# Optimization experiments

Hardware: AMD Instinct MI355X
Metric: run time of the kernel (lower is better)

Reference implementation:

```python
import jax, jax.numpy as jnp
import numpy as np

# constants from init_kwargs (data_info / model_cfg)
FX = 300.0
FY = 300.0
CX = 128.0
CY = 128.0
BG = 1.0            # data_info['bg_color']
EPS2D = 0.3         # gsplat screen-space blur added to 2D covariance diagonal
NEAR = 0.01         # gsplat near-plane cull
C0 = 0.28209479177387814  # SH degree-0 basis
N_PTS = 512
IMG = 256


def quat_to_rotmat(q):
    # q: (N,4) wxyz, normalized inside
    q = q / jnp.linalg.norm(q, axis=-1, keepdims=True)
    w, x, y, z = q[:, 0], q[:, 1], q[:, 2], q[:, 3]
    return jnp.stack([
        jnp.stack([1 - 2 * (y * y + z * z), 2 * (x * y - w * z), 2 * (x * z + w * y)], -1),
        jnp.stack([2 * (x * y + w * z), 1 - 2 * (x * x + z * z), 2 * (y * z - w * x)], -1),
        jnp.stack([2 * (x * z - w * y), 2 * (y * z + w * x), 1 - 2 * (x * x + y * y)], -1),
    ], axis=-2)  # (N,3,3)


def setup_inputs() -> dict:
    key = jax.random.key(0)
    k = jax.random.split(key, 6)
    means = (jax.random.uniform(k[0], (N_PTS, 3), dtype=jnp.float32) - 0.5) * 10.0
    quats = jax.random.normal(k[1], (N_PTS, 4), dtype=jnp.float32)
    # log-scales around 0.2m so Gaussians actually cover pixels
    scales = jnp.log(0.2) + 0.1 * jax.random.normal(k[2], (N_PTS, 3), dtype=jnp.float32)
    opacities = jax.random.normal(k[3], (N_PTS,), dtype=jnp.float32)
    sh0 = 0.5 * jax.random.normal(k[4], (N_PTS, 1, 3), dtype=jnp.float32)
    shN = 0.01 * jax.random.normal(k[5], (N_PTS, 15, 3), dtype=jnp.float32)
    camtoworld = jnp.concatenate([jnp.eye(3, dtype=jnp.float32), jnp.zeros((3, 1), jnp.float32)], axis=1)
    return {"camtoworld": camtoworld, "means": means, "quats": quats, "scales": scales,
            "opacities": opacities, "sh0": sh0, "shN": shN, "img_h": IMG, "img_w": IMG}


def _render(camtoworld, means, quats, scales, opacities, sh0, shN, img_h, img_w):
    # --- camera setup (matches module forward) ---
    c2w = jnp.eye(4, dtype=jnp.float32).at[:3, :].set(camtoworld)
    viewmat = jnp.linalg.inv(c2w)
    viewmat = viewmat.at[1, :].multiply(-1.0).at[2, :].multiply(-1.0)
    R, t = viewmat[:3, :3], viewmat[:3, 3]

    # --- project means ---
    p = means @ R.T + t                      # (N,3) camera-space
    x, y, z = p[:, 0], p[:, 1], p[:, 2]
    valid = z > NEAR
    zs = jnp.where(valid, z, 1.0)
    rz = 1.0 / zs

    # --- 3D covariance: R(q) diag(s^2) R(q)^T, rotated to camera ---
    Rq = quat_to_rotmat(quats)
    M = Rq * jnp.exp(scales)[:, None, :]
    cov3d = M @ jnp.swapaxes(M, 1, 2)        # (N,3,3)
    cov_cam = jnp.einsum('ij,njk,lk->nil', R, cov3d, R)

    # --- EWA perspective Jacobian with fov clipping (gsplat persp_proj) ---
    limx = 1.3 * (0.5 * img_w / FX)
    limy = 1.3 * (0.5 * img_h / FY)
    tx = zs * jnp.clip(x * rz, -limx, limx)
    ty = zs * jnp.clip(y * rz, -limy, limy)
    zero = jnp.zeros_like(rz)
    J = jnp.stack([
        jnp.stack([FX * rz, zero, -FX * tx * rz * rz], -1),
        jnp.stack([zero, FY * rz, -FY * ty * rz * rz], -1),
    ], axis=1)                               # (N,2,3)
    cov2d = jnp.einsum('nij,njk,nlk->nil', J, cov_cam, J)
    a = cov2d[:, 0, 0] + EPS2D
    b = cov2d[:, 0, 1]
    c = cov2d[:, 1, 1] + EPS2D
    det = a * c - b * b
    valid = valid & (det > 1e-12)
    dets = jnp.where(valid, det, 1.0)
    cA, cB, cC = c / dets, -b / dets, a / dets   # conic (inverse 2D covariance)

    mx = FX * x * rz + CX
    my = FY * y * rz + CY

    # --- colors: sh_degree = 0 -> only sh0 band, clamped to >= 0 ---
    color = jnp.maximum(C0 * sh0[:, 0, :] + 0.5, 0.0)   # (N,3)
    opac = jax.nn.sigmoid(opacities)

    # --- depth sort (front to back) ---
    order = jnp.argsort(jnp.where(valid, z, jnp.inf))
    mx, my, cA, cB, cC, opac, color, valid = (v[order] for v in (mx, my, cA, cB, cC, opac, color, valid))

    # --- per-pixel alpha evaluation (dense [N,H,W]) ---
    px = jnp.arange(img_w, dtype=jnp.float32) + 0.5
    py = jnp.arange(img_h, dtype=jnp.float32) + 0.5
    dx = px[None, None, :] - mx[:, None, None]          # (N,H,W)
    dy = py[None, :, None] - my[:, None, None]
    sigma = 0.5 * (cA[:, None, None] * dx * dx + cC[:, None, None] * dy * dy) + cB[:, None, None] * dx * dy
    alpha = jnp.minimum(0.999, opac[:, None, None] * jnp.exp(-sigma))
    alpha = jnp.where((sigma >= 0.0) & (alpha >= 1.0 / 255.0) & valid[:, None, None], alpha, 0.0)

    # --- front-to-back alpha compositing via exclusive cumprod of (1-alpha) ---
    T = jnp.cumprod(1.0 - alpha, axis=0)                # (N,H,W)
    T_excl = jnp.concatenate([jnp.ones_like(T[:1]), T[:-1]], axis=0)
    w = T_excl * alpha
    render = jnp.einsum('nhw,nc->hwc', w, color) + T[-1][..., None] * BG   # (H,W,3)
    alpha_map = (1.0 - T[-1])[..., None]                                   # (H,W,1)
    return render, alpha_map


def reference(camtoworld, means, quats, scales, opacities, sh0, shN, img_h, img_w):
    return _render(camtoworld, means, quats, scales, opacities, sh0, shN, img_h, img_w)
```

## Files before the change

### kernel.cpp

```cpp
#include <hip/hip_runtime.h>
#include <math.h>

#define FXc 300.0f
#define FYc 300.0f
#define CXc 128.0f
#define CYc 128.0f
#define BGc 1.0f
#define EPS2Dc 0.3f
#define NEARc 0.01f
#define C0c 0.28209479177387814f

#define MAXP 512
#define SEG  4

__global__ void __launch_bounds__(1024)
gs_fused(const float* __restrict__ cam,
         const float* __restrict__ means,
         const float* __restrict__ quats,
         const float* __restrict__ scales,
         const float* __restrict__ opacs,
         const float* __restrict__ sh0,
         const int* __restrict__ img_w_p,
         float* __restrict__ out,
         int n, int npix)
{
    __shared__ float4 spts[MAXP][3];
    __shared__ __align__(16) float zc[MAXP + 4];
    __shared__ int scnt[MAXP / 64];
    __shared__ int sbase[MAXP / 64 + 1];
    __shared__ float4 comb[SEG - 1][256];

    const int lt   = threadIdx.x;
    const int wave = lt >> 6;

    const int W = *img_w_p;
    const int tiles_x = W >> 4;
    const int tx = (blockIdx.x % tiles_x) << 4;
    const int ty = (blockIdx.x / tiles_x) << 4;
    const float tx0 = (float)tx + 0.5f, tx1 = (float)tx + 15.5f;
    const float ty0 = (float)ty + 0.5f, ty1 = (float)ty + 15.5f;

    const int nchunks = (n + 63) >> 6;

    float pmx = 0.f, pmy = 0.f, pA_ = 0.f, pB_ = 0.f, pC_ = 0.f;
    float pop = 0.f, pcr = 0.f, pcg = 0.f, pcb = 0.f, pz = 0.f;
    unsigned long long mreg = 0ull;
    bool phit = false;

    if (lt < MAXP) {
        const float a00 = cam[0], a01 = cam[1], a02 = cam[2],  b0 = cam[3];
        const float a10 = cam[4], a11 = cam[5], a12 = cam[6],  b1 = cam[7];
        const float a20 = cam[8], a21 = cam[9], a22 = cam[10], b2 = cam[11];
        const float det3 = a00*(a11*a22 - a12*a21) - a01*(a10*a22 - a12*a20) + a02*(a10*a21 - a11*a20);
        const float id = 1.0f / det3;
        const float i00 = (a11*a22 - a12*a21)*id, i01 = (a02*a21 - a01*a22)*id, i02 = (a01*a12 - a02*a11)*id;
        const float i10 = (a12*a20 - a10*a22)*id, i11 = (a00*a22 - a02*a20)*id, i12 = (a02*a10 - a00*a12)*id;
        const float i20 = (a10*a21 - a11*a20)*id, i21 = (a01*a20 - a00*a21)*id, i22 = (a00*a11 - a01*a10)*id;
        const float R00 = i00,  R01 = i01,  R02 = i02;
        const float R10 = -i10, R11 = -i11, R12 = -i12;
        const float R20 = -i20, R21 = -i21, R22 = -i22;
        const float t0 = -(i00*b0 + i01*b1 + i02*b2);
        const float t1 = (i10*b0 + i11*b1 + i12*b2);
        const float t2 = (i20*b0 + i21*b1 + i22*b2);
        const float limx_e = 1.3f * (0.5f * (float)W / FXc);
        const float limy_e = limx_e;

        const int p = lt;
        bool hit = false;
        if (p < n) {
            const float m0 = means[3*p], m1 = means[3*p+1], m2 = means[3*p+2];
            const float px_ = R00*m0 + R01*m1 + R02*m2 + t0;
            const float py_ = R10*m0 + R11*m1 + R12*m2 + t1;
            const float pz_ = R20*m0 + R21*m1 + R22*m2 + t2;

            bool valid = pz_ > NEARc;
            const float zs = valid ? pz_ : 1.0f;
            const float rz = 1.0f / zs;

            float qw = quats[4*p], qx = quats[4*p+1], qy = quats[4*p+2], qz = quats[4*p+3];
            const float qn = rsqrtf(qw*qw + qx*qx + qy*qy + qz*qz);
            qw *= qn; qx *= qn; qy *= qn; qz *= qn;
            const float Rq00 = 1.f - 2.f*(qy*qy + qz*qz), Rq01 = 2.f*(qx*qy - qw*qz), Rq02 = 2.f*(qx*qz + qw*qy);
            const float Rq10 = 2.f*(qx*qy + qw*qz), Rq11 = 1.f - 2.f*(qx*qx + qz*qz), Rq12 = 2.f*(qy*qz - qw*qx);
            const float Rq20 = 2.f*(qx*qz - qw*qy), Rq21 = 2.f*(qy*qz + qw*qx), Rq22 = 1.f - 2.f*(qx*qx + qy*qy);

            const float e0 = __expf(scales[3*p]), e1 = __expf(scales[3*p+1]), e2 = __expf(scales[3*p+2]);
            const float M00 = Rq00*e0, M01 = Rq01*e1, M02 = Rq02*e2;
            const float M10 = Rq10*e0, M11 = Rq11*e1, M12 = Rq12*e2;
            const float M20 = Rq20*e0, M21 = Rq21*e1, M22 = Rq22*e2;

            const float S00 = M00*M00 + M01*M01 + M02*M02;
            const float S01 = M00*M10 + M01*M11 + M02*M12;
            const float S02 = M00*M20 + M01*M21 + M02*M22;
            const float S11 = M10*M10 + M11*M11 + M12*M12;
            const float S12 = M10*M20 + M11*M21 + M12*M22;
            const float S22 = M20*M20 + M21*M21 + M22*M22;

            const float U00 = R00*S00 + R01*S01 + R02*S02;
            const float U01 = R00*S01 + R01*S11 + R02*S12;
            const float U02 = R00*S02 + R01*S12 + R02*S22;
            const float U10 = R10*S00 + R11*S01 + R12*S02;
            const float U11 = R10*S01 + R11*S11 + R12*S12;
            const float U12 = R10*S02 + R11*S12 + R12*S22;
            const float U20 = R20*S00 + R21*S01 + R22*S02;
            const float U21 = R20*S01 + R21*S11 + R22*S12;
            const float U22 = R20*S02 + R21*S12 + R22*S22;

            const float C00 = U00*R00 + U01*R01 + U02*R02;
            const float C01 = U00*R10 + U01*R11 + U02*R12;
            const float C02 = U00*R20 + U01*R21 + U02*R22;
            const float C11 = U10*R10 + U11*R11 + U12*R12;
            const float C12 = U10*R20 + U11*R21 + U12*R22;
            const float C22 = U20*R20 + U21*R21 + U22*R22;

            const float txc = zs * fminf(fmaxf(px_*rz, -limx_e), limx_e);
            const float tyc = zs * fminf(fmaxf(py_*rz, -limy_e), limy_e);
            const float ja0 = FXc * rz;
            const float ja2 = -FXc * txc * rz * rz;
            const float jb1 = FYc * rz;
            const float jb2 = -FYc * tyc * rz * rz;

            const float c2d00 = ja0*ja0*C00 + 2.f*ja0*ja2*C02 + ja2*ja2*C22 + EPS2Dc;
            const float c2d01 = ja0*jb1*C01 + ja0*jb2*C02 + ja2*jb1*C12 + ja2*jb2*C22;
            const float c2d11 = jb1*jb1*C11 + 2.f*jb1*jb2*C12 + jb2*jb2*C22 + EPS2Dc;

            const float det2 = c2d00*c2d11 - c2d01*c2d01;
            valid = valid && (det2 > 1e-12f);
            const float rdet = 1.0f / (valid ? det2 : 1.0f);
            pA_ = c2d11 * rdet;
            pB_ = -c2d01 * rdet;
            pC_ = c2d00 * rdet;

            pmx = FXc * px_ * rz + CXc;
            pmy = FYc * py_ * rz + CYc;

            pcr = fmaxf(C0c * sh0[3*p+0] + 0.5f, 0.0f);
            pcg = fmaxf(C0c * sh0[3*p+1] + 0.5f, 0.0f);
            pcb = fmaxf(C0c * sh0[3*p+2] + 0.5f, 0.0f);
            pop = 1.0f / (1.0f + __expf(-opacs[p]));
            pz  = pz_;

            if (valid) {
                const float a_ = pA_, b_ = pB_, c_ = pC_;
                const float dx0 = tx0 - pmx, dx1 = tx1 - pmx;
                const float dy0 = ty0 - pmy, dy1 = ty1 - pmy;
                float smin;
                if (dx0 <= 0.f && 0.f <= dx1 && dy0 <= 0.f && 0.f <= dy1) {
                    smin = 0.f;
                } else {
                    const float ra = 1.0f / a_, rc = 1.0f / c_;
                    float yy = fminf(fmaxf(-b_ * dx0 * rc, dy0), dy1);
                    float s0 = 0.5f*a_*dx0*dx0 + b_*dx0*yy + 0.5f*c_*yy*yy;
                    yy = fminf(fmaxf(-b_ * dx1 * rc, dy0), dy1);
                    float s1 = 0.5f*a_*dx1*dx1 + b_*dx1*yy + 0.5f*c_*yy*yy;
                    float xx = fminf(fmaxf(-b_ * dy0 * ra, dx0), dx1);
                    float s2 = 0.5f*a_*xx*xx + b_*xx*dy0 + 0.5f*c_*dy0*dy0;
                    xx = fminf(fmaxf(-b_ * dy1 * ra, dx0), dx1);
                    float s3 = 0.5f*a_*xx*xx + b_*xx*dy1 + 0.5f*c_*dy1*dy1;
                    smin = fminf(fminf(s0, s1), fminf(s2, s3));
                }
                hit = (smin <= __logf(pop * 255.0f) + 1e-3f);
            }
        }
        phit = hit;
        mreg = __ballot(hit);
        if ((lt & 63) == 0) scnt[wave] = __popcll(mreg);
    }
    __syncthreads();

    if (lt == 0) {
        int acc = 0;
        for (int c = 0; c < nchunks; ++c) { sbase[c] = acc; acc += scnt[c]; }
        sbase[nchunks] = acc;
    }
    __syncthreads();
    const int k = sbase[nchunks];

    int pslot = -1;
    if (lt < MAXP && phit) {
        pslot = sbase[wave] + __popcll(mreg & ((1ull << (lt & 63)) - 1ull));
        zc[pslot] = pz;
    }
    if (lt < 4) zc[k + lt] = INFINITY;
    __syncthreads();

    if (pslot >= 0) {
        const float za = pz;
        const int sa = pslot;
        int rank = 0;
        const float4* z4 = (const float4*)zc;
        const int k4 = (k + 3) >> 2;
        for (int j4 = 0; j4 < k4; ++j4) {
            const float4 v = z4[j4];
            const int j = j4 << 2;
            rank += (v.x < za || (v.x == za && (j+0) < sa));
            rank += (v.y < za || (v.y == za && (j+1) < sa));
            rank += (v.z < za || (v.z == za && (j+2) < sa));
            rank += (v.w < za || (v.w == za && (j+3) < sa));
        }
        spts[rank][0] = make_float4(pmx, pmy, pA_, pB_);
        spts[rank][1] = make_float4(pC_, pop, pcr, pcg);
        spts[rank][2] = make_float4(pcb, 0.f, 0.f, 0.f);
    }
    __syncthreads();

    const int s   = lt >> 8;
    const int pix = lt & 255;
    const int col = tx + (pix & 15);
    const int row = ty + (pix >> 4);
    const float px = (float)col + 0.5f;
    const float py = (float)row + 0.5f;

    const int beg = (k * s) >> 2;
    const int end = (k * (s + 1)) >> 2;

    float T = 1.0f, r_ = 0.f, g_ = 0.f, b_ = 0.f;
    for (int base = beg; base < end; base += 8) {
        const int lim = (base + 8 < end) ? base + 8 : end;
        #pragma unroll 8
        for (int i = base; i < lim; ++i) {
            const float4 a4 = spts[i][0];
            const float4 b4 = spts[i][1];
            const float  cbv = spts[i][2].x;

            const float dx = px - a4.x;
            const float dy = py - a4.y;
            const float sigma = 0.5f * (a4.z*dx*dx + b4.x*dy*dy) + a4.w*dx*dy;
            float al = b4.y * __expf(-sigma);
            al = fminf(al, 0.999f);
            const bool keep = (sigma >= 0.0f) && (al >= (1.0f/255.0f));
            al = keep ? al : 0.0f;

            const float w = T * al;
            r_ += w * b4.z;
            g_ += w * b4.w;
            b_ += w * cbv;
            T = __builtin_fmaf(-al, T, T);
        }
        if (!__any(T > 1e-4f)) break;
    }

    if (s > 0) comb[s - 1][pix] = make_float4(r_, g_, b_, T);
    __syncthreads();

    if (s == 0) {
        const float4 f1 = comb[0][pix];
        const float4 f2 = comb[1][pix];
        const float4 f3 = comb[2][pix];
        float rr = r_ + T * (f1.x + f1.w * (f2.x + f2.w * f3.x));
        float gg = g_ + T * (f1.y + f1.w * (f2.y + f2.w * f3.y));
        float bb = b_ + T * (f1.z + f1.w * (f2.z + f2.w * f3.z));
        const float Tt = T * f1.w * f2.w * f3.w;
        rr += Tt * BGc; gg += Tt * BGc; bb += Tt * BGc;

        const int opix = row * W + col;
        if (opix < npix) {
            out[3*opix + 0] = rr;
            out[3*opix + 1] = gg;
            out[3*opix + 2] = bb;
            out[3*npix + opix] = 1.0f - Tt;
        }
    }
}

extern "C" void kernel_launch(void* const* d_in, const int* in_sizes, int n_in,
                              void* d_out, int out_size, void* d_ws, size_t ws_size,
                              hipStream_t stream) {
    const float* cam    = (const float*)d_in[0];
    const float* means  = (const float*)d_in[1];
    const float* quats  = (const float*)d_in[2];
    const float* scales = (const float*)d_in[3];
    const float* opacs  = (const float*)d_in[4];
    const float* sh0    = (const float*)d_in[5];
    const int* img_w = (const int*)d_in[8];

    const int n = in_sizes[4];
    const int npix = out_size / 4;

    const int blocks = npix / 256;
    gs_fused<<<blocks, 1024, 0, stream>>>(cam, means, quats, scales, opacs, sh0,
                                          img_w, (float*)d_out, n, npix);
}
```

Baseline: 10.35 us.

## Split depth list into 8 segments, two pixels per thread, pack colors as bf16

Each thread now shades two pixels eight rows apart, sharing the shared-memory loads of each Gaussian's parameters, and the sorted list is split into eight depth segments instead of four so all 1024 threads stay busy. Red and green are rounded to bf16 and packed into one float, so the per-point record shrinks from three float4 to two. The combine step becomes a loop over seven partial segments. This trades extra registers and some color precision for fewer LDS reads per pixel. Early termination now only fires when both pixels saturate. The npix bound check on the output writes is dropped.

```diff
diff --git a/kernel.cpp b/kernel.cpp
--- a/kernel.cpp
+++ b/kernel.cpp
@@ -11,7 +11,7 @@
 #define C0c 0.28209479177387814f
 
 #define MAXP 512
-#define SEG  4
+#define SEG  8
 
 __global__ void __launch_bounds__(1024)
 gs_fused(const float* __restrict__ cam,
@@ -24,7 +24,7 @@
          float* __restrict__ out,
          int n, int npix)
 {
-    __shared__ float4 spts[MAXP][3];
+    __shared__ float4 spts[MAXP][2];
     __shared__ __align__(16) float zc[MAXP + 4];
     __shared__ int scnt[MAXP / 64];
     __shared__ int sbase[MAXP / 64 + 1];
@@ -198,68 +198,95 @@
             rank += (v.z < za || (v.z == za && (j+2) < sa));
             rank += (v.w < za || (v.w == za && (j+3) < sa));
         }
+        unsigned ur = __float_as_uint(pcr);
+        ur = (ur + 0x7FFFu + ((ur >> 16) & 1u)) & 0xFFFF0000u;
+        unsigned ug = __float_as_uint(pcg);
+        ug = (ug + 0x7FFFu + ((ug >> 16) & 1u)) >> 16;
+        const float crcg = __uint_as_float(ur | ug);
         spts[rank][0] = make_float4(pmx, pmy, pA_, pB_);
-        spts[rank][1] = make_float4(pC_, pop, pcr, pcg);
-        spts[rank][2] = make_float4(pcb, 0.f, 0.f, 0.f);
-    }
-    __syncthreads();
-
-    const int s   = lt >> 8;
-    const int pix = lt & 255;
-    const int col = tx + (pix & 15);
-    const int row = ty + (pix >> 4);
-    const float px = (float)col + 0.5f;
-    const float py = (float)row + 0.5f;
-
-    const int beg = (k * s) >> 2;
-    const int end = (k * (s + 1)) >> 2;
-
-    float T = 1.0f, r_ = 0.f, g_ = 0.f, b_ = 0.f;
-    for (int base = beg; base < end; base += 8) {
-        const int lim = (base + 8 < end) ? base + 8 : end;
-        #pragma unroll 8
+        spts[rank][1] = make_float4(pC_, pop, crcg, pcb);
+    }
+    __syncthreads();
+
+    const int s  = lt >> 7;
+    const int p0 = lt & 127;
+    const int col  = tx + (p0 & 15);
+    const int row0 = ty + (p0 >> 4);
+    const float px  = (float)col + 0.5f;
+    const float py0 = (float)row0 + 0.5f;
+    const float py1 = py0 + 8.0f;
+
+    const int beg = (k * s) >> 3;
+    const int end = (k * (s + 1)) >> 3;
+
+    float T0 = 1.0f, r0 = 0.f, g0 = 0.f, b0 = 0.f;
+    float T1 = 1.0f, r1 = 0.f, g1 = 0.f, b1 = 0.f;
+    for (int base = beg; base < end; base += 4) {
+        const int lim = (base + 4 < end) ? base + 4 : end;
+        #pragma unroll 4
         for (int i = base; i < lim; ++i) {
             const float4 a4 = spts[i][0];
             const float4 b4 = spts[i][1];
-            const float  cbv = spts[i][2].x;
-
-            const float dx = px - a4.x;
-            const float dy = py - a4.y;
-            const float sigma = 0.5f * (a4.z*dx*dx + b4.x*dy*dy) + a4.w*dx*dy;
-            float al = b4.y * __expf(-sigma);
-            al = fminf(al, 0.999f);
-            const bool keep = (sigma >= 0.0f) && (al >= (1.0f/255.0f));
-            al = keep ? al : 0.0f;
-
-            const float w = T * al;
-            r_ += w * b4.z;
-            g_ += w * b4.w;
-            b_ += w * cbv;
-            T = __builtin_fmaf(-al, T, T);
-        }
-        if (!__any(T > 1e-4f)) break;
-    }
-
-    if (s > 0) comb[s - 1][pix] = make_float4(r_, g_, b_, T);
+            const unsigned uc = __float_as_uint(b4.z);
+            const float crf = __uint_as_float(uc & 0xFFFF0000u);
+            const float cgf = __uint_as_float(uc << 16);
+            const float cbv = b4.w;
+
+            const float dx  = px  - a4.x;
+            const float dy0 = py0 - a4.y;
+            const float dy1 = py1 - a4.y;
+
+            const float sg0 = 0.5f * (a4.z*dx*dx + b4.x*dy0*dy0) + a4.w*dx*dy0;
+            float al0 = b4.y * __expf(-sg0);
+            al0 = fminf(al0, 0.999f);
+            al0 = ((sg0 >= 0.0f) && (al0 >= (1.0f/255.0f))) ? al0 : 0.0f;
+            const float w0 = T0 * al0;
+            r0 += w0 * crf; g0 += w0 * cgf; b0 += w0 * cbv;
+            T0 = __builtin_fmaf(-al0, T0, T0);
+
+            const float sg1 = 0.5f * (a4.z*dx*dx + b4.x*dy1*dy1) + a4.w*dx*dy1;
+            float al1 = b4.y * __expf(-sg1);
+            al1 = fminf(al1, 0.999f);
+            al1 = ((sg1 >= 0.0f) && (al1 >= (1.0f/255.0f))) ? al1 : 0.0f;
+            const float w1 = T1 * al1;
+            r1 += w1 * crf; g1 += w1 * cgf; b1 += w1 * cbv;
+            T1 = __builtin_fmaf(-al1, T1, T1);
+        }
+        if (!__any(fmaxf(T0, T1) > 1e-4f)) break;
+    }
+
+    if (s > 0) {
+        comb[s - 1][p0]       = make_float4(r0, g0, b0, T0);
+        comb[s - 1][p0 + 128] = make_float4(r1, g1, b1, T1);
+    }
     __syncthreads();
 
     if (s == 0) {
-        const float4 f1 = comb[0][pix];
-        const float4 f2 = comb[1][pix];
-        const float4 f3 = comb[2][pix];
-        float rr = r_ + T * (f1.x + f1.w * (f2.x + f2.w * f3.x));
-        float gg = g_ + T * (f1.y + f1.w * (f2.y + f2.w * f3.y));
-        float bb = b_ + T * (f1.z + f1.w * (f2.z + f2.w * f3.z));
-        const float Tt = T * f1.w * f2.w * f3.w;
+        float rr = r0, gg = g0, bb = b0, Tt = T0;
+        #pragma unroll
+        for (int ss = 0; ss < SEG - 1; ++ss) {
+            const float4 f = comb[ss][p0];
+            rr += Tt * f.x; gg += Tt * f.y; bb += Tt * f.z; Tt *= f.w;
+        }
         rr += Tt * BGc; gg += Tt * BGc; bb += Tt * BGc;
-
-        const int opix = row * W + col;
-        if (opix < npix) {
-            out[3*opix + 0] = rr;
-            out[3*opix + 1] = gg;
-            out[3*opix + 2] = bb;
-            out[3*npix + opix] = 1.0f - Tt;
-        }
+        int opix = row0 * W + col;
+        out[3*opix + 0] = rr;
+        out[3*opix + 1] = gg;
+        out[3*opix + 2] = bb;
+        out[3*npix + opix] = 1.0f - Tt;
+
+        rr = r1; gg = g1; bb = b1; Tt = T1;
+        #pragma unroll
+        for (int ss = 0; ss < SEG - 1; ++ss) {
+            const float4 f = comb[ss][p0 + 128];
+            rr += Tt * f.x; gg += Tt * f.y; bb += Tt * f.z; Tt *= f.w;
+        }
+        rr += Tt * BGc; gg += Tt * BGc; bb += Tt * BGc;
+        opix = (row0 + 8) * W + col;
+        out[3*opix + 0] = rr;
+        out[3*opix + 1] = gg;
+        out[3*opix + 2] = bb;
+        out[3*npix + opix] = 1.0f - Tt;
     }
 }
 
```

Result: no change. 10.50 us (+1.4%).
